# Optimization experiments

Hardware: AMD Instinct MI355X
Metric: run time of the kernel (lower is better)

## Reference

```python
import jax, jax.numpy as jnp
import numpy as np

NUM_NODES = 20000
NUM_EDGES = 320000
NODE_DIM = 256
EDGE_DIM = 64
HIDDEN = 512

def _glorot(key, shape):
    fan_in = shape[0]
    bound = 1.0 / np.sqrt(fan_in)
    return jax.random.uniform(key, shape, jnp.float32, -bound, bound)

def setup_inputs() -> dict:
    key = jax.random.key(0)
    ks = jax.random.split(key, 12)
    node_features = jax.random.normal(ks[0], (NUM_NODES, NODE_DIM), jnp.float32)
    edge_index = jax.random.randint(ks[1], (2, NUM_EDGES), 0, NUM_NODES, jnp.int64 if jax.config.jax_enable_x64 else jnp.int32)
    edge_features = jax.random.normal(ks[2], (NUM_EDGES, EDGE_DIM), jnp.float32)
    edge_in = 2 * NODE_DIM + EDGE_DIM
    node_in = NODE_DIM + HIDDEN
    params = {
        'W1': _glorot(ks[3], (edge_in, HIDDEN)), 'b1': _glorot(ks[4], (HIDDEN,)),
        'W2': _glorot(ks[5], (HIDDEN, HIDDEN)), 'b2': _glorot(ks[6], (HIDDEN,)),
        'W3': _glorot(ks[7], (node_in, HIDDEN)), 'b3': _glorot(ks[8], (HIDDEN,)),
        'W4': _glorot(ks[9], (HIDDEN, NODE_DIM)), 'b4': _glorot(ks[10], (NODE_DIM,)),
    }
    return {'node_features': node_features, 'edge_index': edge_index,
            'edge_features': edge_features, **params}

def reference(node_features, edge_index, edge_features,
              W1, b1, W2, b2, W3, b3, W4, b4):
    src_idx = edge_index[0]
    tgt_idx = edge_index[1]
    # gather endpoints: [E, 2*node_dim + edge_dim]
    edge_input = jnp.concatenate(
        [node_features[src_idx], node_features[tgt_idx], edge_features], axis=-1)
    # edge MLP
    h = jax.nn.relu(edge_input @ W1 + b1)
    messages = h @ W2 + b2                      # [E, hidden]
    # scatter-add aggregate per target node
    aggregated = jax.ops.segment_sum(messages, tgt_idx, num_segments=NUM_NODES)
    # node MLP + residual
    node_input = jnp.concatenate([node_features, aggregated], axis=-1)
    g = jax.nn.relu(node_input @ W3 + b3)
    node_update = g @ W4 + b4                   # [N, node_dim]
    return node_features + node_update
```

## Files before the change

### kernel.cpp

```cpp
#include <hip/hip_runtime.h>

#define NUM_NODES 20000
#define NUM_EDGES 320000
#define NODE_DIM  256
#define EDGE_DIM  64
#define HIDDEN    512

typedef short  s16x8  __attribute__((ext_vector_type(8)));
typedef float  f32x16 __attribute__((ext_vector_type(16)));
typedef unsigned short us16;

__device__ __forceinline__ us16 f2bf(float f) {
    union { float f; unsigned u; } c; c.f = f;
    unsigned r = c.u + 0x7fffu + ((c.u >> 16) & 1u);
    return (us16)(r >> 16);
}
__device__ __forceinline__ float bf2f(us16 b) {
    union { unsigned u; float f; } c; c.u = ((unsigned)b) << 16;
    return c.f;
}
__device__ __forceinline__ int swapmid(int x) {
    return (x & 3) | ((x & 4) << 1) | ((x & 8) >> 1);
}
__device__ __forceinline__ void zero16(f32x16& a) {
    #pragma unroll
    for (int i = 0; i < 16; ++i) a[i] = 0.0f;
}
__device__ __forceinline__ void mfma3(f32x16& acc, s16x8 ah, s16x8 al, s16x8 bh, s16x8 bl) {
    acc = __builtin_amdgcn_mfma_f32_32x32x16_bf16(ah, bh, acc, 0, 0, 0);
    acc = __builtin_amdgcn_mfma_f32_32x32x16_bf16(ah, bl, acc, 0, 0, 0);
    acc = __builtin_amdgcn_mfma_f32_32x32x16_bf16(al, bh, acc, 0, 0, 0);
}
template<int STRIDE>
__device__ __forceinline__ void stash_quad(char* hi, char* lo, int r, int c, float4 v) {
    int cpp = (c & ~15) | swapmid(c & 15);
    int off = r * STRIDE + ((cpp * 2) ^ ((r & 7) << 4));
    us16 h0 = f2bf(v.x), h1 = f2bf(v.y), h2 = f2bf(v.z), h3 = f2bf(v.w);
    uint2 uh; uh.x = h0 | ((unsigned)h1 << 16); uh.y = h2 | ((unsigned)h3 << 16);
    uint2 ul;
    ul.x = f2bf(v.x - bf2f(h0)) | ((unsigned)f2bf(v.y - bf2f(h1)) << 16);
    ul.y = f2bf(v.z - bf2f(h2)) | ((unsigned)f2bf(v.w - bf2f(h3)) << 16);
    *reinterpret_cast<uint2*>(hi + off) = uh;
    *reinterpret_cast<uint2*>(lo + off) = ul;
}
template<int STRIDE>
__device__ __forceinline__ void bread(const char* hi, const char* lo, int r, int kbyte,
                                      s16x8& bh, s16x8& bl) {
    int off = r * STRIDE + (kbyte ^ ((r & 7) << 4));
    bh = *reinterpret_cast<const s16x8*>(hi + off);
    bl = *reinterpret_cast<const s16x8*>(lo + off);
}

__global__ void build_deg(const int* __restrict__ tgt, int* __restrict__ deg) {
    int i = blockIdx.x * 256 + threadIdx.x;
    if (i < NUM_EDGES) atomicAdd(&deg[tgt[i]], 1);
}

__global__ void scan_deg(const int* __restrict__ deg, int* __restrict__ off) {
    __shared__ int sums[1024];
    const int tid  = threadIdx.x;
    const int base = tid * 20;
    int local[20];
    int s = 0;
    #pragma unroll
    for (int i = 0; i < 20; ++i) {
        local[i] = s;
        int idx = base + i;
        s += (idx < NUM_NODES) ? deg[idx] : 0;
    }
    sums[tid] = s;
    __syncthreads();
    for (int d = 1; d < 1024; d <<= 1) {
        int add = (tid >= d) ? sums[tid - d] : 0;
        __syncthreads();
        sums[tid] += add;
        __syncthreads();
    }
    const int chunk_off = sums[tid] - s;
    #pragma unroll
    for (int i = 0; i < 20; ++i) {
        int idx = base + i;
        if (idx <= NUM_NODES) off[idx] = chunk_off + local[i];
    }
}

__global__ void fill_csr(const int* __restrict__ src, const int* __restrict__ tgt,
                         const int* __restrict__ off,
                         int* __restrict__ cursor, int2* __restrict__ csr2) {
    int i = blockIdx.x * 256 + threadIdx.x;
    if (i < NUM_EDGES) {
        int t = tgt[i];
        int p = atomicAdd(&cursor[t], 1);
        csr2[off[t] + p] = make_int2(i, src[i]);
    }
}

__global__ void compute_w23(const float* __restrict__ W2, const float* __restrict__ b2,
                            const float* __restrict__ W3,
                            float* __restrict__ W23, float* __restrict__ b23) {
    int n = blockIdx.y * 256 + threadIdx.x;
    int i = blockIdx.x;
    const float* w3b = W3 + 256 * 512 + n;
    float s = 0.f;
    if (i < 512) {
        const float* w2r = W2 + i * 512;
        for (int j = 0; j < 512; ++j) s = fmaf(w2r[j], w3b[(size_t)j * 512], s);
        W23[i * 512 + n] = s;
    } else {
        for (int j = 0; j < 512; ++j) s = fmaf(b2[j], w3b[(size_t)j * 512], s);
        b23[n] = s;
    }
}

__global__ void prep_planes(const float* __restrict__ W1, const float* __restrict__ W3,
                            const float* __restrict__ W4, const float* __restrict__ W23,
                            us16* __restrict__ wab_h, us16* __restrict__ wab_l,
                            us16* __restrict__ wc_h,  us16* __restrict__ wc_l,
                            us16* __restrict__ w34_h, us16* __restrict__ w34_l,
                            us16* __restrict__ w4_h,  us16* __restrict__ w4_l) {
    int idx = blockIdx.x * 256 + threadIdx.x;
    float w; us16 *dh, *dl; int k, n, N;
    if (idx < 262144) {
        n = idx & 1023; k = idx >> 10; N = 1024;
        w = W1[(k + (n >= 512 ? 256 : 0)) * 512 + (n & 511)];
        dh = wab_h; dl = wab_l;
    } else if (idx < 294912) {
        int j = idx - 262144; n = j & 511; k = j >> 9; N = 512;
        w = W1[(512 + k) * 512 + n];
        dh = wc_h; dl = wc_l;
    } else if (idx < 688128) {
        int j = idx - 294912; n = j & 511; k = j >> 9; N = 512;
        w = (k < 256) ? W3[k * 512 + n] : W23[(k - 256) * 512 + n];
        dh = w34_h; dl = w34_l;
    } else {
        int j = idx - 688128; n = j & 255; k = j >> 8; N = 256;
        w = W4[k * 256 + n];
        dh = w4_h; dl = w4_l;
    }
    us16 h = f2bf(w);
    us16 l = f2bf(w - bf2f(h));
    int d = (k >> 4) * (N * 16) + n * 16 + swapmid(k & 15);
    dh[d] = h; dl[d] = l;
}

__global__ __launch_bounds__(512, 2)
void gemm_p(const float* __restrict__ nf,
            const us16* __restrict__ wab_h, const us16* __restrict__ wab_l,
            float* __restrict__ P) {
    extern __shared__ char sB[];
    const int tid = threadIdx.x;
    const int nb  = blockIdx.x * 64;
    const int half = blockIdx.y;

    const float4* nf4 = reinterpret_cast<const float4*>(nf);
    for (int i = tid; i < 64 * 64; i += 512) {
        int r = i >> 6, q = i & 63;
        int row = nb + r; if (row >= NUM_NODES) row = NUM_NODES - 1;
        stash_quad<512>(sB, sB + 32768, r, 4 * q, nf4[(size_t)row * 64 + q]);
    }
    __syncthreads();

    const int w = tid >> 6, l = tid & 63, le = l & 31, g = l >> 5;
    const s16x8* Ah = reinterpret_cast<const s16x8*>(wab_h);
    const s16x8* Al = reinterpret_cast<const s16x8*>(wab_l);
    const int nbase = half * 512 + w * 64;

    f32x16 acc[2][2];
    #pragma unroll
    for (int a = 0; a < 2; ++a) { zero16(acc[a][0]); zero16(acc[a][1]); }

    for (int ks = 0; ks < 16; ++ks) {
        s16x8 AH[2], AL[2], bh[2], bl[2];
        #pragma unroll
        for (int mt = 0; mt < 2; ++mt) {
            int idx = ks * 2048 + (nbase + 32 * mt + le) * 2 + g;
            AH[mt] = Ah[idx]; AL[mt] = Al[idx];
        }
        #pragma unroll
        for (int rt = 0; rt < 2; ++rt)
            bread<512>(sB, sB + 32768, 32 * rt + le, ks * 32 + 16 * g, bh[rt], bl[rt]);
        #pragma unroll
        for (int mt = 0; mt < 2; ++mt)
            #pragma unroll
            for (int rt = 0; rt < 2; ++rt)
                mfma3(acc[mt][rt], AH[mt], AL[mt], bh[rt], bl[rt]);
    }

    float4* P4 = reinterpret_cast<float4*>(P);
    #pragma unroll
    for (int rt = 0; rt < 2; ++rt) {
        int row = nb + 32 * rt + le;
        if (row < NUM_NODES) {
            #pragma unroll
            for (int mt = 0; mt < 2; ++mt)
                #pragma unroll
                for (int rq = 0; rq < 4; ++rq) {
                    int nn = nbase + 32 * mt + 4 * g + 8 * rq;
                    float4 o = make_float4(acc[mt][rt][4*rq+0], acc[mt][rt][4*rq+1],
                                           acc[mt][rt][4*rq+2], acc[mt][rt][4*rq+3]);
                    P4[(size_t)row * 256 + (nn >> 2)] = o;
                }
        }
    }
}

__global__ __launch_bounds__(512, 4)
void edge_csr(const int2* __restrict__ csr2, const int* __restrict__ offs,
              const float* __restrict__ ef,
              const us16* __restrict__ wc_h, const us16* __restrict__ wc_l,
              const float* __restrict__ b1, const float* __restrict__ P,
              float* __restrict__ aggH) {
    extern __shared__ char dsm[];
    char* sC = dsm;
    char* sB = dsm + 65536;
    __shared__ int sOff[5];

    const int tid  = threadIdx.x;
    const int orig = blockIdx.x;
    const int wg   = (orig & 7) * 625 + (orig >> 3);
    const int t0   = wg * 4;

    if (tid < 5) sOff[tid] = offs[t0 + tid];
    __syncthreads();

    const int ebase = sOff[0];
    const int eend  = sOff[4];
    const int L     = eend - ebase;
    const int nwin  = (L + 31) >> 5;

    const float4* ef4 = reinterpret_cast<const float4*>(ef);
    const float4* P4  = reinterpret_cast<const float4*>(P);
    const float4* b14 = reinterpret_cast<const float4*>(b1);
    const int w = tid >> 6, l = tid & 63, le = l & 31, g = l >> 5;
    const int grp = tid >> 7, slice = tid & 127;
    const int tg  = t0 + grp;
    const int tlo = sOff[grp], thi = sOff[grp + 1];
    const s16x8* Ah = reinterpret_cast<const s16x8*>(wc_h);
    const s16x8* Al = reinterpret_cast<const s16x8*>(wc_l);

    const float4 pt = P4[(size_t)tg * 256 + 128 + slice];
    float4 sum = make_float4(0.f, 0.f, 0.f, 0.f);

    for (int win = 0; win < nwin; ++win) {
        const int wbase = ebase + (win << 5);
        {
            const int se = tid >> 4, sq = tid & 15;
            int p  = wbase + se;
            int pc = (p < eend) ? p : ebase;
            int eid = csr2[pc].x;
            stash_quad<128>(sB, sB + 4096, se, 4 * sq, ef4[(size_t)eid * 16 + sq]);
        }
        __syncthreads();

        #pragma unroll
        for (int mt = 0; mt < 2; ++mt) {
            f32x16 acc; zero16(acc);
            #pragma unroll
            for (int ks = 0; ks < 4; ++ks) {
                int idx = ks * 1024 + (w * 64 + 32 * mt + le) * 2 + g;
                s16x8 bh, bl;
                bread<128>(sB, sB + 4096, le, ks * 32 + 16 * g, bh, bl);
                mfma3(acc, Ah[idx], Al[idx], bh, bl);
            }
            #pragma unroll
            for (int rq = 0; rq < 4; ++rq) {
                int h0 = w * 64 + 32 * mt + 4 * g + 8 * rq;
                float4 bq = b14[h0 >> 2];
                float4 v = make_float4(acc[4*rq+0] + bq.x, acc[4*rq+1] + bq.y,
                                       acc[4*rq+2] + bq.z, acc[4*rq+3] + bq.w);
                *reinterpret_cast<float4*>(sC + le * 2048 + ((h0 * 4) ^ ((le & 15) << 4))) = v;
            }
        }
        __syncthreads();

        {
            const int lo = (tlo > wbase) ? tlo : wbase;
            const int hi = (thi < wbase + 32) ? thi : (wbase + 32);
            for (int base = lo; base < hi; base += 8) {
                const int m = (hi - base < 8) ? (hi - base) : 8;
                int srcv[8];
                #pragma unroll
                for (int j = 0; j < 8; ++j)
                    srcv[j] = csr2[base + ((j < m) ? j : 0)].y;
                float4 pa[8];
                #pragma unroll
                for (int j = 0; j < 8; ++j)
                    pa[j] = P4[(size_t)srcv[j] * 256 + slice];
                #pragma unroll
                for (int j = 0; j < 8; ++j) {
                    if (j < m) {
                        int crow = (base + j) - wbase;
                        float4 c = *reinterpret_cast<const float4*>(
                            sC + crow * 2048 + ((slice * 16) ^ ((crow & 15) << 4)));
                        sum.x += fmaxf(pa[j].x + pt.x + c.x, 0.f);
                        sum.y += fmaxf(pa[j].y + pt.y + c.y, 0.f);
                        sum.z += fmaxf(pa[j].z + pt.z + c.z, 0.f);
                        sum.w += fmaxf(pa[j].w + pt.w + c.w, 0.f);
                    }
                }
            }
        }
        __syncthreads();
    }

    *reinterpret_cast<float4*>(aggH + (size_t)tg * 512 + slice * 4) = sum;
}

__global__ __launch_bounds__(512, 2)
void node_mlp(const float* __restrict__ nf, const float* __restrict__ aggH,
              const int* __restrict__ deg,
              const us16* __restrict__ w34_h, const us16* __restrict__ w34_l,
              const us16* __restrict__ w4_h,  const us16* __restrict__ w4_l,
              const float* __restrict__ b3, const float* __restrict__ b23,
              const float* __restrict__ b4, float* __restrict__ out) {
    extern __shared__ char sm[];
    __shared__ int sDeg[32];
    const int tid = threadIdx.x;
    const int nb  = blockIdx.x * 32;

    if (tid < 32) sDeg[tid] = deg[nb + tid];

    const float4* nf4 = reinterpret_cast<const float4*>(nf);
    const float4* ag4 = reinterpret_cast<const float4*>(aggH);
    auto stage = [&](int c, char* buf) {
        for (int i = tid; i < 32 * 64; i += 512) {
            int r = i >> 6, q = i & 63;
            float4 v = (c == 0) ? nf4[(size_t)(nb + r) * 64 + q]
                                : ag4[(size_t)(nb + r) * 128 + (c - 1) * 64 + q];
            stash_quad<512>(buf, buf + 16384, r, 4 * q, v);
        }
    };

    stage(0, sm);
    __syncthreads();

    const int w = tid >> 6, l = tid & 63, le = l & 31, g = l >> 5;

    f32x16 acc[2]; zero16(acc[0]); zero16(acc[1]);
    {
        const s16x8* Ah = reinterpret_cast<const s16x8*>(w34_h);
        const s16x8* Al = reinterpret_cast<const s16x8*>(w34_l);
        #pragma unroll
        for (int c = 0; c < 3; ++c) {
            char* cur = sm + (c & 1) * 32768;
            char* oth = sm + ((c + 1) & 1) * 32768;
            if (c < 2) stage(c + 1, oth);
            #pragma unroll
            for (int ksl = 0; ksl < 16; ++ksl) {
                int ks = c * 16 + ksl;
                s16x8 AH[2], AL[2], bh, bl;
                #pragma unroll
                for (int mt = 0; mt < 2; ++mt) {
                    int idx = ks * 1024 + (w * 64 + 32 * mt + le) * 2 + g;
                    AH[mt] = Ah[idx]; AL[mt] = Al[idx];
                }
                bread<512>(cur, cur + 16384, le, ksl * 32 + 16 * g, bh, bl);
                #pragma unroll
                for (int mt = 0; mt < 2; ++mt) mfma3(acc[mt], AH[mt], AL[mt], bh, bl);
            }
            __syncthreads();
        }
    }

    {
        const float4* b34  = reinterpret_cast<const float4*>(b3);
        const float4* b234 = reinterpret_cast<const float4*>(b23);
        const float degv = (float)sDeg[le];
        #pragma unroll
        for (int mt = 0; mt < 2; ++mt)
            #pragma unroll
            for (int rq = 0; rq < 4; ++rq) {
                int hcol = w * 64 + 32 * mt + 4 * g + 8 * rq;
                float4 bq = b34[hcol >> 2], cq = b234[hcol >> 2];
                float4 gv;
                gv.x = fmaxf(acc[mt][4*rq+0] + bq.x + degv * cq.x, 0.f);
                gv.y = fmaxf(acc[mt][4*rq+1] + bq.y + degv * cq.y, 0.f);
                gv.z = fmaxf(acc[mt][4*rq+2] + bq.z + degv * cq.z, 0.f);
                gv.w = fmaxf(acc[mt][4*rq+3] + bq.w + degv * cq.w, 0.f);
                stash_quad<1024>(sm, sm + 32768, le, hcol, gv);
            }
    }
    __syncthreads();

    f32x16 a2; zero16(a2);
    {
        const s16x8* Ah = reinterpret_cast<const s16x8*>(w4_h);
        const s16x8* Al = reinterpret_cast<const s16x8*>(w4_l);
        for (int ks = 0; ks < 32; ++ks) {
            s16x8 AH, AL, bh, bl;
            int idx = ks * 512 + (w * 32 + le) * 2 + g;
            AH = Ah[idx]; AL = Al[idx];
            bread<1024>(sm, sm + 32768, le, ks * 32 + 16 * g, bh, bl);
            mfma3(a2, AH, AL, bh, bl);
        }
    }

    const float4* b44 = reinterpret_cast<const float4*>(b4);
    float4* out4 = reinterpret_cast<float4*>(out);
    #pragma unroll
    for (int rq = 0; rq < 4; ++rq) {
        int n0 = w * 32 + 4 * g + 8 * rq;
        float4 bq  = b44[n0 >> 2];
        float4 res = nf4[(size_t)(nb + le) * 64 + (n0 >> 2)];
        float4 o;
        o.x = res.x + a2[4*rq+0] + bq.x;
        o.y = res.y + a2[4*rq+1] + bq.y;
        o.z = res.z + a2[4*rq+2] + bq.z;
        o.w = res.w + a2[4*rq+3] + bq.w;
        out4[(size_t)(nb + le) * 64 + (n0 >> 2)] = o;
    }
}

extern "C" void kernel_launch(void* const* d_in, const int* in_sizes, int n_in,
                              void* d_out, int out_size, void* d_ws, size_t ws_size,
                              hipStream_t stream) {
    const float* nf = (const float*)d_in[0];
    const int*   ei = (const int*)d_in[1];
    const float* ef = (const float*)d_in[2];
    const float* W1 = (const float*)d_in[3];
    const float* b1 = (const float*)d_in[4];
    const float* W2 = (const float*)d_in[5];
    const float* b2 = (const float*)d_in[6];
    const float* W3 = (const float*)d_in[7];
    const float* b3 = (const float*)d_in[8];
    const float* W4 = (const float*)d_in[9];
    const float* b4 = (const float*)d_in[10];
    float* out = (float*)d_out;

    char* ws = (char*)d_ws;
    float* P      = (float*)(ws + 0);
    float* aggH   = (float*)(ws + 81920000);
    us16*  wab_h  = (us16*)(ws + 122880000);
    us16*  wab_l  = (us16*)(ws + 123404288);
    us16*  wc_h   = (us16*)(ws + 123928576);
    us16*  wc_l   = (us16*)(ws + 123994112);
    us16*  w34_h  = (us16*)(ws + 124059648);
    us16*  w34_l  = (us16*)(ws + 124846080);
    us16*  w4_h   = (us16*)(ws + 125632512);
    us16*  w4_l   = (us16*)(ws + 125894656);
    float* W23    = (float*)(ws + 126156800);
    float* b23    = (float*)(ws + 127205376);
    int*   deg    = (int*)  (ws + 127207424);
    int*   cursor = (int*)  (ws + 127287424);
    int*   offs   = (int*)  (ws + 127367424);
    int2*  csr2   = (int2*) (ws + 127447440);

    const int* src = ei;
    const int* tgt = ei + NUM_EDGES;

    (void)hipFuncSetAttribute(reinterpret_cast<const void*>(&edge_csr),
                              hipFuncAttributeMaxDynamicSharedMemorySize, 73728);
    (void)hipFuncSetAttribute(reinterpret_cast<const void*>(&node_mlp),
                              hipFuncAttributeMaxDynamicSharedMemorySize, 65536);
    (void)hipFuncSetAttribute(reinterpret_cast<const void*>(&gemm_p),
                              hipFuncAttributeMaxDynamicSharedMemorySize, 65536);

    hipMemsetAsync(deg, 0, 160000, stream);

    build_deg<<<1250, 256, 0, stream>>>(tgt, deg);
    scan_deg<<<1, 1024, 0, stream>>>(deg, offs);
    fill_csr<<<1250, 256, 0, stream>>>(src, tgt, offs, cursor, csr2);

    compute_w23<<<dim3(513, 2), 256, 0, stream>>>(W2, b2, W3, W23, b23);
    prep_planes<<<3200, 256, 0, stream>>>(W1, W3, W4, W23,
                                          wab_h, wab_l, wc_h, wc_l,
                                          w34_h, w34_l, w4_h, w4_l);

    gemm_p<<<dim3(313, 2), 512, 65536, stream>>>(nf, wab_h, wab_l, P);
    edge_csr<<<5000, 512, 73728, stream>>>(csr2, offs, ef, wc_h, wc_l, b1, P, aggH);
    node_mlp<<<625, 512, 65536, stream>>>(nf, aggH, deg, w34_h, w34_l,
                                          w4_h, w4_l, b3, b23, b4, out);
}
```

Before: 931.0 us.

## Balance edge aggregation across thread groups by window slots instead of target node

Previously each 128-thread group handled only the edges of its own target node within each 32-edge window, so groups idled when degrees were uneven. Now each group processes a fixed 8 edges of every window, selecting the target's P slice and a per-target accumulator through a slot index. Source ids and slots are staged in shared memory, and a final shared-memory reduction combines the four partial sums per target. This trades extra registers, branchy accumulator selection and a final reduction for even load across groups and fewer redundant csr reads.

After: 1.038 ms. 11.5% more time.

```diff
diff --git a/kernel.cpp b/kernel.cpp
--- a/kernel.cpp
+++ b/kernel.cpp
@@ -214,6 +214,8 @@
     char* sC = dsm;
     char* sB = dsm + 65536;
     __shared__ int sOff[5];
+    __shared__ int sSrcW[32];
+    __shared__ int sSlotW[32];
 
     const int tid  = threadIdx.x;
     const int orig = blockIdx.x;
@@ -225,24 +227,31 @@
 
     const int ebase = sOff[0];
     const int eend  = sOff[4];
-    const int L     = eend - ebase;
-    const int nwin  = (L + 31) >> 5;
+    const int nwin  = (eend - ebase + 31) >> 5;
+    const int o1 = sOff[1], o2 = sOff[2], o3 = sOff[3];
 
     const float4* ef4 = reinterpret_cast<const float4*>(ef);
     const float4* P4  = reinterpret_cast<const float4*>(P);
     const float4* b14 = reinterpret_cast<const float4*>(b1);
     const int w = tid >> 6, l = tid & 63, le = l & 31, g = l >> 5;
     const int grp = tid >> 7, slice = tid & 127;
-    const int tg  = t0 + grp;
-    const int tlo = sOff[grp], thi = sOff[grp + 1];
     const s16x8* Ah = reinterpret_cast<const s16x8*>(wc_h);
     const s16x8* Al = reinterpret_cast<const s16x8*>(wc_l);
 
-    const float4 pt = P4[(size_t)tg * 256 + 128 + slice];
-    float4 sum = make_float4(0.f, 0.f, 0.f, 0.f);
+    float4 pt0 = P4[(size_t)(t0 + 0) * 256 + 128 + slice];
+    float4 pt1 = P4[(size_t)(t0 + 1) * 256 + 128 + slice];
+    float4 pt2 = P4[(size_t)(t0 + 2) * 256 + 128 + slice];
+    float4 pt3 = P4[(size_t)(t0 + 3) * 256 + 128 + slice];
+    float4 s0 = make_float4(0.f,0.f,0.f,0.f), s1 = s0, s2 = s0, s3 = s0;
 
     for (int win = 0; win < nwin; ++win) {
         const int wbase = ebase + (win << 5);
+        if (tid < 32) {
+            int p  = wbase + tid;
+            int pc = (p < eend) ? p : ebase;
+            sSrcW[tid]  = csr2[pc].y;
+            sSlotW[tid] = ((p >= o1) ? 1 : 0) + ((p >= o2) ? 1 : 0) + ((p >= o3) ? 1 : 0);
+        }
         {
             const int se = tid >> 4, sq = tid & 15;
             int p  = wbase + se;
@@ -273,37 +282,55 @@
         }
         __syncthreads();
 
-        {
-            const int lo = (tlo > wbase) ? tlo : wbase;
-            const int hi = (thi < wbase + 32) ? thi : (wbase + 32);
-            for (int base = lo; base < hi; base += 8) {
-                const int m = (hi - base < 8) ? (hi - base) : 8;
-                int srcv[8];
-                #pragma unroll
-                for (int j = 0; j < 8; ++j)
-                    srcv[j] = csr2[base + ((j < m) ? j : 0)].y;
-                float4 pa[8];
-                #pragma unroll
-                for (int j = 0; j < 8; ++j)
-                    pa[j] = P4[(size_t)srcv[j] * 256 + slice];
-                #pragma unroll
-                for (int j = 0; j < 8; ++j) {
-                    if (j < m) {
-                        int crow = (base + j) - wbase;
-                        float4 c = *reinterpret_cast<const float4*>(
-                            sC + crow * 2048 + ((slice * 16) ^ ((crow & 15) << 4)));
-                        sum.x += fmaxf(pa[j].x + pt.x + c.x, 0.f);
-                        sum.y += fmaxf(pa[j].y + pt.y + c.y, 0.f);
-                        sum.z += fmaxf(pa[j].z + pt.z + c.z, 0.f);
-                        sum.w += fmaxf(pa[j].w + pt.w + c.w, 0.f);
-                    }
+        #pragma unroll
+        for (int b = 0; b < 2; ++b) {
+            const int wi0 = 8 * grp + 4 * b;
+            float4 pa[4];
+            #pragma unroll
+            for (int j = 0; j < 4; ++j)
+                pa[j] = P4[(size_t)sSrcW[wi0 + j] * 256 + slice];
+            #pragma unroll
+            for (int j = 0; j < 4; ++j) {
+                const int widx = wi0 + j;
+                if (wbase + widx < eend) {
+                    const int sl = sSlotW[widx];
+                    float4 ptv = (sl == 0) ? pt0 : (sl == 1) ? pt1 : (sl == 2) ? pt2 : pt3;
+                    float4 c = *reinterpret_cast<const float4*>(
+                        sC + widx * 2048 + ((slice * 16) ^ ((widx & 15) << 4)));
+                    float4 v;
+                    v.x = fmaxf(pa[j].x + ptv.x + c.x, 0.f);
+                    v.y = fmaxf(pa[j].y + ptv.y + c.y, 0.f);
+                    v.z = fmaxf(pa[j].z + ptv.z + c.z, 0.f);
+                    v.w = fmaxf(pa[j].w + ptv.w + c.w, 0.f);
+                    if      (sl == 0) { s0.x += v.x; s0.y += v.y; s0.z += v.z; s0.w += v.w; }
+                    else if (sl == 1) { s1.x += v.x; s1.y += v.y; s1.z += v.z; s1.w += v.w; }
+                    else if (sl == 2) { s2.x += v.x; s2.y += v.y; s2.z += v.z; s2.w += v.w; }
+                    else              { s3.x += v.x; s3.y += v.y; s3.z += v.z; s3.w += v.w; }
                 }
             }
         }
         __syncthreads();
     }
 
-    *reinterpret_cast<float4*>(aggH + (size_t)tg * 512 + slice * 4) = sum;
+    float4* part = reinterpret_cast<float4*>(dsm);
+    part[(grp * 4 + 0) * 128 + slice] = s0;
+    part[(grp * 4 + 1) * 128 + slice] = s1;
+    part[(grp * 4 + 2) * 128 + slice] = s2;
+    part[(grp * 4 + 3) * 128 + slice] = s3;
+    __syncthreads();
+    {
+        const int tslot = grp;
+        float4 a = part[(0 * 4 + tslot) * 128 + slice];
+        float4 b = part[(1 * 4 + tslot) * 128 + slice];
+        float4 c = part[(2 * 4 + tslot) * 128 + slice];
+        float4 d = part[(3 * 4 + tslot) * 128 + slice];
+        float4 o;
+        o.x = (a.x + b.x) + (c.x + d.x);
+        o.y = (a.y + b.y) + (c.y + d.y);
+        o.z = (a.z + b.z) + (c.z + d.z);
+        o.w = (a.w + b.w) + (c.w + d.w);
+        *reinterpret_cast<float4*>(aggH + (size_t)(t0 + tslot) * 512 + slice * 4) = o;
+    }
 }
 
 __global__ __launch_bounds__(512, 2)
```

## Split edge work into per-target 32-edge chunks with atomic merge

Applied to the files above, without the earlier changes.

Replaces the fixed four-targets-per-block edge kernel with a chunked schedule: each block handles one chunk of up to 32 edges of a single target node, built from a second scan over ceil(deg/32). The target projection is folded into the MFMA epilogue, and the four row-group partials are reduced in shared memory. Targets with several chunks merge via float atomics into a pre-zeroed aggH. This is meant to remove load imbalance and the wasted window padding of the old grouping. In exchange it launches a fixed 30000-block grid where surplus blocks exit early, adds extra scan, chunk-fill and memset passes, and adds atomics.

Result: faster. 873.4 us (-6.2%).

```diff
diff --git a/kernel.cpp b/kernel.cpp
--- a/kernel.cpp
+++ b/kernel.cpp
@@ -5,6 +5,7 @@
 #define NODE_DIM  256
 #define EDGE_DIM  64
 #define HIDDEN    512
+#define NCMAX     30000
 
 typedef short  s16x8  __attribute__((ext_vector_type(8)));
 typedef float  f32x16 __attribute__((ext_vector_type(16)));
@@ -56,7 +57,8 @@
     if (i < NUM_EDGES) atomicAdd(&deg[tgt[i]], 1);
 }
 
-__global__ void scan_deg(const int* __restrict__ deg, int* __restrict__ off) {
+template<int SHIFT>
+__global__ void scan_kernel(const int* __restrict__ deg, int* __restrict__ off) {
     __shared__ int sums[1024];
     const int tid  = threadIdx.x;
     const int base = tid * 20;
@@ -66,7 +68,8 @@
     for (int i = 0; i < 20; ++i) {
         local[i] = s;
         int idx = base + i;
-        s += (idx < NUM_NODES) ? deg[idx] : 0;
+        int v = (idx < NUM_NODES) ? deg[idx] : 0;
+        s += (SHIFT == 0) ? v : ((v + 31) >> 5);
     }
     sums[tid] = s;
     __syncthreads();
@@ -92,6 +95,21 @@
         int t = tgt[i];
         int p = atomicAdd(&cursor[t], 1);
         csr2[off[t] + p] = make_int2(i, src[i]);
+    }
+}
+
+__global__ void fill_chunks(const int* __restrict__ deg, const int* __restrict__ offs,
+                            const int* __restrict__ choff, int4* __restrict__ cinfo) {
+    int t = blockIdx.x * 256 + threadIdx.x;
+    if (t < NUM_NODES) {
+        int d = deg[t];
+        int nch = (d + 31) >> 5;
+        int base = choff[t];
+        for (int c = 0; c < nch; ++c) {
+            int rem = d - (c << 5);
+            cinfo[base + c] = make_int4(offs[t] + (c << 5), (rem < 32) ? rem : 32,
+                                        t, (nch > 1) ? 1 : 0);
+        }
     }
 }
 
@@ -205,105 +223,105 @@
 }
 
 __global__ __launch_bounds__(512, 4)
-void edge_csr(const int2* __restrict__ csr2, const int* __restrict__ offs,
-              const float* __restrict__ ef,
-              const us16* __restrict__ wc_h, const us16* __restrict__ wc_l,
-              const float* __restrict__ b1, const float* __restrict__ P,
-              float* __restrict__ aggH) {
+void edge_chunk(const int2* __restrict__ csr2, const int4* __restrict__ cinfo,
+                const int* __restrict__ ncp, const float* __restrict__ ef,
+                const us16* __restrict__ wc_h, const us16* __restrict__ wc_l,
+                const float* __restrict__ b1, const float* __restrict__ P,
+                float* __restrict__ aggH) {
     extern __shared__ char dsm[];
     char* sC = dsm;
     char* sB = dsm + 65536;
-    __shared__ int sOff[5];
-
-    const int tid  = threadIdx.x;
+    __shared__ int sSrcW[32];
+
+    const int NC   = *ncp;
     const int orig = blockIdx.x;
-    const int wg   = (orig & 7) * 625 + (orig >> 3);
-    const int t0   = wg * 4;
-
-    if (tid < 5) sOff[tid] = offs[t0 + tid];
-    __syncthreads();
-
-    const int ebase = sOff[0];
-    const int eend  = sOff[4];
-    const int L     = eend - ebase;
-    const int nwin  = (L + 31) >> 5;
-
+    const int wg   = (orig & 7) * (NCMAX / 8) + (orig >> 3);
+    if (wg >= NC) return;
+
+    const int4 ci = cinfo[wg];
+    const int estart = ci.x, len = ci.y, tg = ci.z, multi = ci.w;
+
+    const int tid = threadIdx.x;
     const float4* ef4 = reinterpret_cast<const float4*>(ef);
     const float4* P4  = reinterpret_cast<const float4*>(P);
     const float4* b14 = reinterpret_cast<const float4*>(b1);
     const int w = tid >> 6, l = tid & 63, le = l & 31, g = l >> 5;
     const int grp = tid >> 7, slice = tid & 127;
-    const int tg  = t0 + grp;
-    const int tlo = sOff[grp], thi = sOff[grp + 1];
     const s16x8* Ah = reinterpret_cast<const s16x8*>(wc_h);
     const s16x8* Al = reinterpret_cast<const s16x8*>(wc_l);
 
-    const float4 pt = P4[(size_t)tg * 256 + 128 + slice];
+    if (tid < 32) sSrcW[tid] = csr2[estart + ((tid < len) ? tid : (len - 1))].y;
+    {
+        const int se = tid >> 4, sq = tid & 15;
+        int p = estart + ((se < len) ? se : (len - 1));
+        int eid = csr2[p].x;
+        stash_quad<128>(sB, sB + 4096, se, 4 * sq, ef4[(size_t)eid * 16 + sq]);
+    }
+    __syncthreads();
+
+    #pragma unroll
+    for (int mt = 0; mt < 2; ++mt) {
+        f32x16 acc; zero16(acc);
+        #pragma unroll
+        for (int ks = 0; ks < 4; ++ks) {
+            int idx = ks * 1024 + (w * 64 + 32 * mt + le) * 2 + g;
+            s16x8 bh, bl;
+            bread<128>(sB, sB + 4096, le, ks * 32 + 16 * g, bh, bl);
+            mfma3(acc, Ah[idx], Al[idx], bh, bl);
+        }
+        #pragma unroll
+        for (int rq = 0; rq < 4; ++rq) {
+            int h0 = w * 64 + 32 * mt + 4 * g + 8 * rq;
+            float4 bq  = b14[h0 >> 2];
+            float4 ptq = P4[(size_t)tg * 256 + 128 + (h0 >> 2)];
+            float4 v = make_float4(acc[4*rq+0] + bq.x + ptq.x, acc[4*rq+1] + bq.y + ptq.y,
+                                   acc[4*rq+2] + bq.z + ptq.z, acc[4*rq+3] + bq.w + ptq.w);
+            *reinterpret_cast<float4*>(sC + le * 2048 + ((h0 * 4) ^ ((le & 15) << 4))) = v;
+        }
+    }
+    __syncthreads();
+
     float4 sum = make_float4(0.f, 0.f, 0.f, 0.f);
-
-    for (int win = 0; win < nwin; ++win) {
-        const int wbase = ebase + (win << 5);
-        {
-            const int se = tid >> 4, sq = tid & 15;
-            int p  = wbase + se;
-            int pc = (p < eend) ? p : ebase;
-            int eid = csr2[pc].x;
-            stash_quad<128>(sB, sB + 4096, se, 4 * sq, ef4[(size_t)eid * 16 + sq]);
-        }
-        __syncthreads();
-
-        #pragma unroll
-        for (int mt = 0; mt < 2; ++mt) {
-            f32x16 acc; zero16(acc);
-            #pragma unroll
-            for (int ks = 0; ks < 4; ++ks) {
-                int idx = ks * 1024 + (w * 64 + 32 * mt + le) * 2 + g;
-                s16x8 bh, bl;
-                bread<128>(sB, sB + 4096, le, ks * 32 + 16 * g, bh, bl);
-                mfma3(acc, Ah[idx], Al[idx], bh, bl);
+    #pragma unroll
+    for (int b = 0; b < 2; ++b) {
+        const int wi0 = 8 * grp + 4 * b;
+        float4 pa[4];
+        #pragma unroll
+        for (int j = 0; j < 4; ++j) {
+            if (wi0 + j < len)
+                pa[j] = P4[(size_t)sSrcW[wi0 + j] * 256 + slice];
+        }
+        #pragma unroll
+        for (int j = 0; j < 4; ++j) {
+            const int s = wi0 + j;
+            if (s < len) {
+                float4 c = *reinterpret_cast<const float4*>(
+                    sC + s * 2048 + ((slice * 16) ^ ((s & 15) << 4)));
+                sum.x += fmaxf(pa[j].x + c.x, 0.f);
+                sum.y += fmaxf(pa[j].y + c.y, 0.f);
+                sum.z += fmaxf(pa[j].z + c.z, 0.f);
+                sum.w += fmaxf(pa[j].w + c.w, 0.f);
             }
-            #pragma unroll
-            for (int rq = 0; rq < 4; ++rq) {
-                int h0 = w * 64 + 32 * mt + 4 * g + 8 * rq;
-                float4 bq = b14[h0 >> 2];
-                float4 v = make_float4(acc[4*rq+0] + bq.x, acc[4*rq+1] + bq.y,
-                                       acc[4*rq+2] + bq.z, acc[4*rq+3] + bq.w);
-                *reinterpret_cast<float4*>(sC + le * 2048 + ((h0 * 4) ^ ((le & 15) << 4))) = v;
-            }
-        }
-        __syncthreads();
-
-        {
-            const int lo = (tlo > wbase) ? tlo : wbase;
-            const int hi = (thi < wbase + 32) ? thi : (wbase + 32);
-            for (int base = lo; base < hi; base += 8) {
-                const int m = (hi - base < 8) ? (hi - base) : 8;
-                int srcv[8];
-                #pragma unroll
-                for (int j = 0; j < 8; ++j)
-                    srcv[j] = csr2[base + ((j < m) ? j : 0)].y;
-                float4 pa[8];
-                #pragma unroll
-                for (int j = 0; j < 8; ++j)
-                    pa[j] = P4[(size_t)srcv[j] * 256 + slice];
-                #pragma unroll
-                for (int j = 0; j < 8; ++j) {
-                    if (j < m) {
-                        int crow = (base + j) - wbase;
-                        float4 c = *reinterpret_cast<const float4*>(
-                            sC + crow * 2048 + ((slice * 16) ^ ((crow & 15) << 4)));
-                        sum.x += fmaxf(pa[j].x + pt.x + c.x, 0.f);
-                        sum.y += fmaxf(pa[j].y + pt.y + c.y, 0.f);
-                        sum.z += fmaxf(pa[j].z + pt.z + c.z, 0.f);
-                        sum.w += fmaxf(pa[j].w + pt.w + c.w, 0.f);
-                    }
-                }
-            }
-        }
-        __syncthreads();
-    }
-
-    *reinterpret_cast<float4*>(aggH + (size_t)tg * 512 + slice * 4) = sum;
+        }
+    }
+    __syncthreads();
+    float4* part = reinterpret_cast<float4*>(dsm);
+    part[grp * 128 + slice] = sum;
+    __syncthreads();
+
+    if (tid < 128) {
+        float4 a = part[0 * 128 + tid], b = part[1 * 128 + tid];
+        float4 c = part[2 * 128 + tid], d = part[3 * 128 + tid];
+        float4 o = make_float4((a.x + b.x) + (c.x + d.x), (a.y + b.y) + (c.y + d.y),
+                               (a.z + b.z) + (c.z + d.z), (a.w + b.w) + (c.w + d.w));
+        float* dst = aggH + (size_t)tg * 512 + tid * 4;
+        if (multi) {
+            atomicAdd(dst + 0, o.x); atomicAdd(dst + 1, o.y);
+            atomicAdd(dst + 2, o.z); atomicAdd(dst + 3, o.w);
+        } else {
+            *reinterpret_cast<float4*>(dst) = o;
+        }
+    }
 }
 
 __global__ __launch_bounds__(512, 2)
@@ -444,11 +462,13 @@
     int*   cursor = (int*)  (ws + 127287424);
     int*   offs   = (int*)  (ws + 127367424);
     int2*  csr2   = (int2*) (ws + 127447440);
+    int*   choff  = (int*)  (ws + 130007440);
+    int4*  cinfo  = (int4*) (ws + 130087456);
 
     const int* src = ei;
     const int* tgt = ei + NUM_EDGES;
 
-    (void)hipFuncSetAttribute(reinterpret_cast<const void*>(&edge_csr),
+    (void)hipFuncSetAttribute(reinterpret_cast<const void*>(&edge_chunk),
                               hipFuncAttributeMaxDynamicSharedMemorySize, 73728);
     (void)hipFuncSetAttribute(reinterpret_cast<const void*>(&node_mlp),
                               hipFuncAttributeMaxDynamicSharedMemorySize, 65536);
@@ -456,10 +476,13 @@
                               hipFuncAttributeMaxDynamicSharedMemorySize, 65536);
 
     hipMemsetAsync(deg, 0, 160000, stream);
+    hipMemsetAsync(aggH, 0, (size_t)NUM_NODES * HIDDEN * 4, stream);
 
     build_deg<<<1250, 256, 0, stream>>>(tgt, deg);
-    scan_deg<<<1, 1024, 0, stream>>>(deg, offs);
+    scan_kernel<0><<<1, 1024, 0, stream>>>(deg, offs);
+    scan_kernel<5><<<1, 1024, 0, stream>>>(deg, choff);
     fill_csr<<<1250, 256, 0, stream>>>(src, tgt, offs, cursor, csr2);
+    fill_chunks<<<79, 256, 0, stream>>>(deg, offs, choff, cinfo);
 
     compute_w23<<<dim3(513, 2), 256, 0, stream>>>(W2, b2, W3, W23, b23);
     prep_planes<<<3200, 256, 0, stream>>>(W1, W3, W4, W23,
@@ -467,7 +490,8 @@
                                           w34_h, w34_l, w4_h, w4_l);
 
     gemm_p<<<dim3(313, 2), 512, 65536, stream>>>(nf, wab_h, wab_l, P);
-    edge_csr<<<5000, 512, 73728, stream>>>(csr2, offs, ef, wc_h, wc_l, b1, P, aggH);
+    edge_chunk<<<NCMAX, 512, 73728, stream>>>(csr2, cinfo, &choff[NUM_NODES],
+                                              ef, wc_h, wc_l, b1, P, aggH);
     node_mlp<<<625, 512, 65536, stream>>>(nf, aggH, deg, w34_h, w34_l,
                                           w4_h, w4_l, b3, b23, b4, out);
 }
```
